# Kernel optimization log

Measured on AMD Instinct MI355X. Metric: run time of the kernel, lower is better.

## Reference

```python
import jax, jax.numpy as jnp
import numpy as np

N_USERS, N_ITEMS = 100000, 100000
N_NODES = N_USERS + N_ITEMS
N_EDGES = 4000000
USER_DIM, ITEM_DIM = 256, 128
COMMON, HIDDEN, OUT = 64, 64, 32


def setup_inputs() -> dict:
    key = jax.random.key(0)
    ks = jax.random.split(key, 12)
    inp = {
        "user_tensor": jax.random.normal(ks[0], (N_USERS, USER_DIM), jnp.float32),
        "item_tensor": jax.random.normal(ks[1], (N_ITEMS, ITEM_DIM), jnp.float32),
        "edge_index": jax.random.randint(ks[2], (2, N_EDGES), 0, N_NODES, jnp.int64),
        "edge_weight": jax.random.uniform(ks[3], (N_EDGES,), jnp.float32),
        # user_proj / item_proj (nn.Linear: y = x @ W + b)
        "Wu": jax.random.normal(ks[4], (USER_DIM, COMMON), jnp.float32) / np.sqrt(USER_DIM),
        "bu": jnp.zeros((COMMON,), jnp.float32),
        "Wi": jax.random.normal(ks[5], (ITEM_DIM, COMMON), jnp.float32) / np.sqrt(ITEM_DIM),
        "bi": jnp.zeros((COMMON,), jnp.float32),
        # GCNConv layers (linear without bias + separate bias)
        "W1": jax.random.normal(ks[6], (COMMON, HIDDEN), jnp.float32) / np.sqrt(COMMON),
        "b1": jnp.zeros((HIDDEN,), jnp.float32),
        "W2": jax.random.normal(ks[7], (HIDDEN, OUT), jnp.float32) / np.sqrt(HIDDEN),
        "b2": jnp.zeros((OUT,), jnp.float32),
    }
    return inp


def gcn_conv(x, W, b, src, dst, ew, num_nodes):
    """PyG GCNConv: add self-loops (weight 1), symmetric deg norm, transform, scatter-add."""
    x = x @ W  # transform first: [N, out]
    loop = jnp.arange(num_nodes, dtype=src.dtype)
    src2 = jnp.concatenate([src, loop])
    dst2 = jnp.concatenate([dst, loop])
    ew2 = jnp.concatenate([ew, jnp.ones((num_nodes,), x.dtype)])
    deg = jax.ops.segment_sum(ew2, dst2, num_segments=num_nodes)
    dinv = jnp.where(deg > 0, jax.lax.rsqrt(deg), 0.0)
    norm = dinv[src2] * ew2 * dinv[dst2]  # [E+N]
    msgs = x[src2] * norm[:, None]  # gather + scale: [E+N, out]
    return jax.ops.segment_sum(msgs, dst2, num_segments=num_nodes) + b


def reference(user_tensor, item_tensor, edge_index, edge_weight,
              Wu, bu, Wi, bi, W1, b1, W2, b2):
    user_emb = user_tensor @ Wu + bu
    item_emb = item_tensor @ Wi + bi
    x = jnp.concatenate([user_emb, item_emb], axis=0)  # [N_NODES, COMMON]
    src, dst = edge_index[0], edge_index[1]
    x = gcn_conv(x, W1, b1, src, dst, edge_weight, N_NODES)
    x = jax.nn.relu(x)
    x = gcn_conv(x, W2, b2, src, dst, edge_weight, N_NODES)
    return x
```

## Files before the change

kernel.cpp:

```cpp
#include <hip/hip_runtime.h>
#include <hip/hip_bf16.h>

#define N_USERS_C 100000
#define N_ITEMS_C 100000
#define N_NODES_C 200000
#define USER_DIM_C 256
#define ITEM_DIM_C 128
#define COMMON_C 64
#define HIDDEN_C 64
#define OUT_DIM_C 32

#define BUCKET_BITS 6
#define BUCKET_NODES 64
#define NBKT (N_NODES_C / BUCKET_NODES)
#define BKT_CAP 1536

#define BIN_GRID 512
#define BIN_CHUNK_MAX 8192
#define MAX_EPT 8

typedef unsigned int uint32;
typedef __bf16 bf16x8 __attribute__((ext_vector_type(8)));
typedef float f32x4 __attribute__((ext_vector_type(4)));



__device__ __forceinline__ float bf2f(ushort u) { return __uint_as_float(((unsigned)u) << 16); }
__device__ __forceinline__ ushort f2bf(float f) {
    unsigned u = __float_as_uint(f);
    return (ushort)((u + 0x7FFFu + ((u >> 16) & 1u)) >> 16);
}
__device__ __forceinline__ void store4(float* p, float a, float b, float c, float d) {
    *(float4*)p = make_float4(a, b, c, d);
}
__device__ __forceinline__ void store4(ushort* p, float a, float b, float c, float d) {
    ushort4 u;
    u.x = f2bf(a); u.y = f2bf(b); u.z = f2bf(c); u.w = f2bf(d);
    *(ushort4*)p = u;
}

union ABFrag {
    uint4 q;
    ushort u[8];
    bf16x8 v;
};


__global__ __launch_bounds__(1024) void bin_kernel(const int* __restrict__ src,
                                                   const int* __restrict__ dst,
                                                   const float* __restrict__ ew,
                                                   int* __restrict__ bucket_cnt,
                                                   uint32* __restrict__ rec, int E, int chunk) {
    __shared__ int hist[NBKT];
    __shared__ int cur[NBKT];
    for (int i = threadIdx.x; i < NBKT; i += 1024) hist[i] = 0;
    __syncthreads();
    const int beg = blockIdx.x * chunk;
    const int end = min(E, beg + chunk);

    int dc[MAX_EPT];
#pragma unroll
    for (int s = 0; s < MAX_EPT / 4; ++s) {
        const int e0 = beg + (threadIdx.x << 2) + (s << 12);
        int4 d4 = make_int4(-1, -1, -1, -1);
        if (e0 + 3 < end) {
            d4 = *(const int4*)(dst + e0);
        } else if (e0 < end) {
            d4.x = dst[e0];
            if (e0 + 1 < end) d4.y = dst[e0 + 1];
            if (e0 + 2 < end) d4.z = dst[e0 + 2];
        }
        dc[s * 4 + 0] = d4.x; dc[s * 4 + 1] = d4.y;
        dc[s * 4 + 2] = d4.z; dc[s * 4 + 3] = d4.w;
        if (d4.x >= 0) atomicAdd(&hist[d4.x >> BUCKET_BITS], 1);
        if (d4.y >= 0) atomicAdd(&hist[d4.y >> BUCKET_BITS], 1);
        if (d4.z >= 0) atomicAdd(&hist[d4.z >> BUCKET_BITS], 1);
        if (d4.w >= 0) atomicAdd(&hist[d4.w >> BUCKET_BITS], 1);
    }
    __syncthreads();

    for (int i = threadIdx.x; i < NBKT; i += 1024) {
        const int h = hist[i];
        cur[i] = h ? atomicAdd(&bucket_cnt[i], h) : 0;
    }
    __syncthreads();

#pragma unroll
    for (int s = 0; s < MAX_EPT / 4; ++s) {
        const int e0 = beg + (threadIdx.x << 2) + (s << 12);
        if (e0 >= end) continue;
        int4 s4;
        float4 w4;
        if (e0 + 3 < end) {
            s4 = *(const int4*)(src + e0);
            w4 = *(const float4*)(ew + e0);
        } else {
            s4 = make_int4(0, 0, 0, 0);
            w4 = make_float4(0, 0, 0, 0);
            s4.x = src[e0]; w4.x = ew[e0];
            if (e0 + 1 < end) { s4.y = src[e0 + 1]; w4.y = ew[e0 + 1]; }
            if (e0 + 2 < end) { s4.z = src[e0 + 2]; w4.z = ew[e0 + 2]; }
        }
        const int dv[4] = {dc[s * 4 + 0], dc[s * 4 + 1], dc[s * 4 + 2], dc[s * 4 + 3]};
        const int sv[4] = {s4.x, s4.y, s4.z, s4.w};
        const float wv[4] = {w4.x, w4.y, w4.z, w4.w};
#pragma unroll
        for (int k = 0; k < 4; ++k) {
            const int d = dv[k];
            if (d < 0) continue;
            uint32 q = (uint32)(wv[k] * 255.0f + 0.5f);
            if (q > 255u) q = 255u;
            const int b = d >> BUCKET_BITS;
            const int slot = atomicAdd(&cur[b], 1);
            if (slot < BKT_CAP)
                rec[(size_t)b * BKT_CAP + slot] =
                    (((uint32)sv[k]) << 14) | (q << 6) | (uint32)(d & (BUCKET_NODES - 1));
        }
    }
}


__global__ void bucket_build_kernel(const uint32* __restrict__ rec,
                                    const int* __restrict__ bucket_cnt,
                                    uint32* __restrict__ csr, int* __restrict__ row_beg,
                                    int* __restrict__ row_cnt, float* __restrict__ dinv) {
    __shared__ int pk[BUCKET_NODES];
    __shared__ int s[BUCKET_NODES];
    __shared__ int cur[BUCKET_NODES];
    const int b = blockIdx.x;
    const int node0 = b << BUCKET_BITS;
    int total = bucket_cnt[b];
    if (total > BKT_CAP) total = BKT_CAP;
    const uint32* r = rec + (size_t)b * BKT_CAP;
    if (threadIdx.x < BUCKET_NODES) pk[threadIdx.x] = 0;
    __syncthreads();
    for (int j0 = threadIdx.x * 4; j0 < total; j0 += 1024) {
        if (j0 + 4 <= total) {
            uint4 r4 = *(const uint4*)(r + j0);
            atomicAdd(&pk[r4.x & (BUCKET_NODES - 1)], (int)((1u << 20) | ((r4.x >> 6) & 255u)));
            atomicAdd(&pk[r4.y & (BUCKET_NODES - 1)], (int)((1u << 20) | ((r4.y >> 6) & 255u)));
            atomicAdd(&pk[r4.z & (BUCKET_NODES - 1)], (int)((1u << 20) | ((r4.z >> 6) & 255u)));
            atomicAdd(&pk[r4.w & (BUCKET_NODES - 1)], (int)((1u << 20) | ((r4.w >> 6) & 255u)));
        } else {
            for (int j = j0; j < total; ++j) {
                uint32 e = r[j];
                atomicAdd(&pk[e & (BUCKET_NODES - 1)], (int)((1u << 20) | ((e >> 6) & 255u)));
            }
        }
    }
    __syncthreads();
    int v = 0;
    if (threadIdx.x < BUCKET_NODES) {
        v = pk[threadIdx.x] >> 20;
        s[threadIdx.x] = v;
    }
    __syncthreads();
#pragma unroll
    for (int off = 1; off < BUCKET_NODES; off <<= 1) {
        int t = (threadIdx.x < BUCKET_NODES && threadIdx.x >= off) ? s[threadIdx.x - off] : 0;
        __syncthreads();
        if (threadIdx.x < BUCKET_NODES) s[threadIdx.x] += t;
        __syncthreads();
    }
    if (threadIdx.x < BUCKET_NODES) {
        const int ex = s[threadIdx.x] - v;
        const int node = node0 + threadIdx.x;
        const int abs0 = b * BKT_CAP + ex;
        row_beg[node] = abs0;
        row_cnt[node] = v;
        dinv[node] = rsqrtf(1.0f + (float)(pk[threadIdx.x] & 0xFFFFF) * (1.0f / 255.0f));
        cur[threadIdx.x] = abs0;
    }
    __syncthreads();
    for (int j0 = threadIdx.x * 4; j0 < total; j0 += 1024) {
        if (j0 + 4 <= total) {
            uint4 r4 = *(const uint4*)(r + j0);
            csr[atomicAdd(&cur[r4.x & (BUCKET_NODES - 1)], 1)] = r4.x;
            csr[atomicAdd(&cur[r4.y & (BUCKET_NODES - 1)], 1)] = r4.y;
            csr[atomicAdd(&cur[r4.z & (BUCKET_NODES - 1)], 1)] = r4.z;
            csr[atomicAdd(&cur[r4.w & (BUCKET_NODES - 1)], 1)] = r4.w;
        } else {
            for (int j = j0; j < total; ++j) {
                uint32 e = r[j];
                csr[atomicAdd(&cur[e & (BUCKET_NODES - 1)], 1)] = e;
            }
        }
    }
}


__device__ __forceinline__ void wt_one(const float* W, ushort* WT, int K, int N, int i) {
    int k = i / N, n = i % N;
    WT[(size_t)n * K + k] = f2bf(W[i]);
}

__global__ void wt_prep_kernel(const float* __restrict__ Wu, const float* __restrict__ Wi,
                               const float* __restrict__ W1, const float* __restrict__ W2,
                               ushort* __restrict__ wtU, ushort* __restrict__ wtI,
                               ushort* __restrict__ wt1, ushort* __restrict__ wt2) {
    const int SU = USER_DIM_C * 64, SI = ITEM_DIM_C * 64, S1 = 64 * 64, S2 = 64 * 32;
    int i = blockIdx.x * blockDim.x + threadIdx.x;
    if (i < SU) { wt_one(Wu, wtU, USER_DIM_C, 64, i); return; }
    i -= SU;
    if (i < SI) { wt_one(Wi, wtI, ITEM_DIM_C, 64, i); return; }
    i -= SI;
    if (i < S1) { wt_one(W1, wt1, 64, 64, i); return; }
    i -= S1;
    if (i < S2) wt_one(W2, wt2, 64, 32, i);
}

template <int K, int NT, bool XF32, bool SCALE>
__global__ __launch_bounds__(256) void mfma_proj_kernel(const void* __restrict__ Xv,
                                                        const ushort* __restrict__ WT,
                                                        const float* __restrict__ bias,
                                                        const float* __restrict__ dinvp,
                                                        ushort* __restrict__ Y, int M) {
    const int lane = threadIdx.x & 63;
    const int wave = threadIdx.x >> 6;
    const int lr = lane & 15;
    const int quad = lane >> 4;
    const int m0 = blockIdx.x * 64 + wave * 16;
    const int N = NT * 16;

    f32x4 acc[NT];
#pragma unroll
    for (int nt = 0; nt < NT; ++nt) acc[nt] = (f32x4){0.0f, 0.0f, 0.0f, 0.0f};

    int arow = m0 + lr;
    if (arow >= M) arow = M - 1;
    const size_t abase = (size_t)arow * K;

    for (int kc = 0; kc < K; kc += 32) {
        const int k0 = kc + quad * 8;
        ABFrag a;
        if (XF32) {
            const float* Xf = (const float*)Xv;
            float4 x0 = *(const float4*)(Xf + abase + k0);
            float4 x1 = *(const float4*)(Xf + abase + k0 + 4);
            a.u[0] = f2bf(x0.x); a.u[1] = f2bf(x0.y); a.u[2] = f2bf(x0.z); a.u[3] = f2bf(x0.w);
            a.u[4] = f2bf(x1.x); a.u[5] = f2bf(x1.y); a.u[6] = f2bf(x1.z); a.u[7] = f2bf(x1.w);
        } else {
            const ushort* Xb = (const ushort*)Xv;
            a.q = *(const uint4*)(Xb + abase + k0);
        }
#pragma unroll
        for (int nt = 0; nt < NT; ++nt) {
            ABFrag bf;
            bf.q = *(const uint4*)(WT + (size_t)(nt * 16 + lr) * K + k0);
            acc[nt] = __builtin_amdgcn_mfma_f32_16x16x32_bf16(a.v, bf.v, acc[nt], 0, 0, 0);
        }
    }

#pragma unroll
    for (int r = 0; r < 4; ++r) {
        const int m = m0 + quad * 4 + r;
        if (m < M) {
            const float sc = SCALE ? dinvp[m] : 1.0f;
#pragma unroll
            for (int nt = 0; nt < NT; ++nt) {
                const int n = nt * 16 + lr;
                const float bc = bias ? bias[n] : 0.0f;
                Y[(size_t)m * N + n] = f2bf((acc[nt][r] + bc) * sc);
            }
        }
    }
}

template <int N, bool RELU, typename TY>
__global__ void gather_kernel(const int* __restrict__ row_beg, const int* __restrict__ row_cnt,
                              const uint32* __restrict__ csr, const ushort* __restrict__ y,
                              const float* __restrict__ dinv, const float* __restrict__ b,
                              TY* __restrict__ out) {
    constexpr int LPN = N / 4;
    const int node = blockIdx.x * (256 / LPN) + threadIdx.x / LPN;
    const int c0 = (threadIdx.x % LPN) * 4;

    const int beg = row_beg[node];
    const int end = beg + row_cnt[node];

    float a0[4] = {0, 0, 0, 0}, a1[4] = {0, 0, 0, 0}, a2[4] = {0, 0, 0, 0}, a3[4] = {0, 0, 0, 0};
    int j = beg;
    for (; j + 4 <= end; j += 4) {
        uint32 e0 = csr[j], e1 = csr[j + 1], e2 = csr[j + 2], e3 = csr[j + 3];
        int s0 = e0 >> 14, s1 = e1 >> 14, s2 = e2 >> 14, s3 = e3 >> 14;
        float c0v = (float)((e0 >> 6) & 255u) * (1.0f / 255.0f);
        float c1v = (float)((e1 >> 6) & 255u) * (1.0f / 255.0f);
        float c2v = (float)((e2 >> 6) & 255u) * (1.0f / 255.0f);
        float c3v = (float)((e3 >> 6) & 255u) * (1.0f / 255.0f);
        ushort4 u0 = *(const ushort4*)(y + (size_t)s0 * N + c0);
        ushort4 u1 = *(const ushort4*)(y + (size_t)s1 * N + c0);
        ushort4 u2 = *(const ushort4*)(y + (size_t)s2 * N + c0);
        ushort4 u3 = *(const ushort4*)(y + (size_t)s3 * N + c0);
        a0[0] += bf2f(u0.x) * c0v; a0[1] += bf2f(u0.y) * c0v;
        a0[2] += bf2f(u0.z) * c0v; a0[3] += bf2f(u0.w) * c0v;
        a1[0] += bf2f(u1.x) * c1v; a1[1] += bf2f(u1.y) * c1v;
        a1[2] += bf2f(u1.z) * c1v; a1[3] += bf2f(u1.w) * c1v;
        a2[0] += bf2f(u2.x) * c2v; a2[1] += bf2f(u2.y) * c2v;
        a2[2] += bf2f(u2.z) * c2v; a2[3] += bf2f(u2.w) * c2v;
        a3[0] += bf2f(u3.x) * c3v; a3[1] += bf2f(u3.y) * c3v;
        a3[2] += bf2f(u3.z) * c3v; a3[3] += bf2f(u3.w) * c3v;
    }
    for (; j < end; ++j) {
        uint32 e = csr[j];
        int s = e >> 14;
        float cv = (float)((e >> 6) & 255u) * (1.0f / 255.0f);
        ushort4 u = *(const ushort4*)(y + (size_t)s * N + c0);
        a0[0] += bf2f(u.x) * cv; a0[1] += bf2f(u.y) * cv;
        a0[2] += bf2f(u.z) * cv; a0[3] += bf2f(u.w) * cv;
    }
    const float di = dinv[node];
    ushort4 us = *(const ushort4*)(y + (size_t)node * N + c0);
    float4 bc = *(const float4*)(b + c0);
    float r0 = (((a0[0] + a1[0]) + (a2[0] + a3[0])) + bf2f(us.x)) * di + bc.x;
    float r1 = (((a0[1] + a1[1]) + (a2[1] + a3[1])) + bf2f(us.y)) * di + bc.y;
    float r2 = (((a0[2] + a1[2]) + (a2[2] + a3[2])) + bf2f(us.z)) * di + bc.z;
    float r3 = (((a0[3] + a1[3]) + (a2[3] + a3[3])) + bf2f(us.w)) * di + bc.w;
    if (RELU) {
        r0 = fmaxf(r0, 0.0f); r1 = fmaxf(r1, 0.0f);
        r2 = fmaxf(r2, 0.0f); r3 = fmaxf(r3, 0.0f);
    }
    store4(&out[(size_t)node * N + c0], r0, r1, r2, r3);
}


extern "C" void kernel_launch(void* const* d_in, const int* in_sizes, int n_in,
                              void* d_out, int out_size, void* d_ws, size_t ws_size,
                              hipStream_t stream) {
    const float* user = (const float*)d_in[0];
    const float* item = (const float*)d_in[1];
    const int* ei = (const int*)d_in[2];
    const float* ew = (const float*)d_in[3];
    const float* Wu = (const float*)d_in[4];
    const float* bu = (const float*)d_in[5];
    const float* Wi = (const float*)d_in[6];
    const float* bi = (const float*)d_in[7];
    const float* W1 = (const float*)d_in[8];
    const float* b1 = (const float*)d_in[9];
    const float* W2 = (const float*)d_in[10];
    const float* b2 = (const float*)d_in[11];
    float* out = (float*)d_out;

    const int E = in_sizes[3];
    const int* src = ei;
    const int* dst = ei + E;
    const int NB = N_NODES_C;
    const int nblk = (E > BIN_GRID * BIN_CHUNK_MAX) ? ((E + BIN_CHUNK_MAX - 1) / BIN_CHUNK_MAX)
                                                    : BIN_GRID;
    const int chunk = (((E + nblk - 1) / nblk) + 3) & ~3;

    char* p = (char*)d_ws;
    uint32* rec = (uint32*)p;  p += (size_t)NBKT * BKT_CAP * 4;
    uint32* csr = (uint32*)p;  p += (size_t)NBKT * BKT_CAP * 4;
    ushort* emb = (ushort*)p;  p += (size_t)NB * 64 * 2;
    ushort* y1 = (ushort*)p;   p += (size_t)NB * 64 * 2;
    ushort* h1 = (ushort*)p;   p += (size_t)NB * 64 * 2;
    ushort* y2 = (ushort*)p;   p += (size_t)NB * 32 * 2;
    int* bucket_cnt = (int*)p; p += (size_t)NBKT * 4;
    int* row_beg = (int*)p;    p += (size_t)NB * 4;
    int* row_cnt = (int*)p;    p += (size_t)NB * 4;
    float* dinv = (float*)p;   p += (size_t)NB * 4;
    ushort* wtU = (ushort*)p;  p += (size_t)USER_DIM_C * 64 * 2;
    ushort* wtI = (ushort*)p;  p += (size_t)ITEM_DIM_C * 64 * 2;
    ushort* wt1 = (ushort*)p;  p += (size_t)64 * 64 * 2;
    ushort* wt2 = (ushort*)p;  p += (size_t)64 * 32 * 2;

    hipMemsetAsync(bucket_cnt, 0, (size_t)NBKT * 4, stream);
    bin_kernel<<<nblk, 1024, 0, stream>>>(src, dst, ew, bucket_cnt, rec, E, chunk);
    bucket_build_kernel<<<NBKT, 256, 0, stream>>>(rec, bucket_cnt, csr, row_beg, row_cnt, dinv);

    wt_prep_kernel<<<120, 256, 0, stream>>>(Wu, Wi, W1, W2, wtU, wtI, wt1, wt2);

    mfma_proj_kernel<USER_DIM_C, 4, true, false><<<(N_USERS_C + 63) / 64, 256, 0, stream>>>(
        user, wtU, bu, nullptr, emb, N_USERS_C);
    mfma_proj_kernel<ITEM_DIM_C, 4, true, false><<<(N_ITEMS_C + 63) / 64, 256, 0, stream>>>(
        item, wtI, bi, nullptr, emb + (size_t)N_USERS_C * 64, N_ITEMS_C);

    mfma_proj_kernel<64, 4, false, true><<<NB / 64, 256, 0, stream>>>(
        emb, wt1, (const float*)nullptr, dinv, y1, NB);
    gather_kernel<64, true><<<NB / 16, 256, 0, stream>>>(row_beg, row_cnt, csr, y1, dinv, b1, h1);

    mfma_proj_kernel<64, 2, false, true><<<NB / 64, 256, 0, stream>>>(
        h1, wt2, (const float*)nullptr, dinv, y2, NB);
    gather_kernel<32, false><<<NB / 32, 256, 0, stream>>>(row_beg, row_cnt, csr, y2, dinv, b2, out);
}
```

Baseline: 540.4 us.

## Use 256-node coarse buckets with in-place register-staged CSR build

Dst bucketing moves from 64-node to 256-node buckets, so the binning kernel's shared histogram shrinks and there are fewer global bucket atomics. Records become 8-byte pairs (src<<8|q, dst). The build kernel keeps each bucket's records in registers and then writes the packed 32-bit CSR over the same buffer, which drops the separate CSR allocation. This reduces shared-memory pressure and the number of build blocks. In exchange, binning writes twice as many bytes, and per-bucket overflow handling depends on the new capacity.

```diff
diff --git a/kernel.cpp b/kernel.cpp
--- a/kernel.cpp
+++ b/kernel.cpp
@@ -10,10 +10,12 @@
 #define HIDDEN_C 64
 #define OUT_DIM_C 32
 
-#define BUCKET_BITS 6
-#define BUCKET_NODES 64
-#define NBKT (N_NODES_C / BUCKET_NODES)
-#define BKT_CAP 1536
+#define CB_BITS 8
+#define CB_NODES 256
+#define NCB ((N_NODES_C + CB_NODES - 1) / CB_NODES)
+#define CB_CAP 5632
+#define B_THREADS 256
+#define B_UNROLL (CB_CAP / B_THREADS)
 
 #define BIN_GRID 512
 #define BIN_CHUNK_MAX 8192
@@ -50,10 +52,10 @@
                                                    const int* __restrict__ dst,
                                                    const float* __restrict__ ew,
                                                    int* __restrict__ bucket_cnt,
-                                                   uint32* __restrict__ rec, int E, int chunk) {
-    __shared__ int hist[NBKT];
-    __shared__ int cur[NBKT];
-    for (int i = threadIdx.x; i < NBKT; i += 1024) hist[i] = 0;
+                                                   uint2* __restrict__ rec2, int E, int chunk) {
+    __shared__ int hist[NCB];
+    __shared__ int cur[NCB];
+    for (int i = threadIdx.x; i < NCB; i += 1024) hist[i] = 0;
     __syncthreads();
     const int beg = blockIdx.x * chunk;
     const int end = min(E, beg + chunk);
@@ -72,14 +74,14 @@
         }
         dc[s * 4 + 0] = d4.x; dc[s * 4 + 1] = d4.y;
         dc[s * 4 + 2] = d4.z; dc[s * 4 + 3] = d4.w;
-        if (d4.x >= 0) atomicAdd(&hist[d4.x >> BUCKET_BITS], 1);
-        if (d4.y >= 0) atomicAdd(&hist[d4.y >> BUCKET_BITS], 1);
-        if (d4.z >= 0) atomicAdd(&hist[d4.z >> BUCKET_BITS], 1);
-        if (d4.w >= 0) atomicAdd(&hist[d4.w >> BUCKET_BITS], 1);
-    }
-    __syncthreads();
-
-    for (int i = threadIdx.x; i < NBKT; i += 1024) {
+        if (d4.x >= 0) atomicAdd(&hist[d4.x >> CB_BITS], 1);
+        if (d4.y >= 0) atomicAdd(&hist[d4.y >> CB_BITS], 1);
+        if (d4.z >= 0) atomicAdd(&hist[d4.z >> CB_BITS], 1);
+        if (d4.w >= 0) atomicAdd(&hist[d4.w >> CB_BITS], 1);
+    }
+    __syncthreads();
+
+    for (int i = threadIdx.x; i < NCB; i += 1024) {
         const int h = hist[i];
         cur[i] = h ? atomicAdd(&bucket_cnt[i], h) : 0;
     }
@@ -110,80 +112,74 @@
             if (d < 0) continue;
             uint32 q = (uint32)(wv[k] * 255.0f + 0.5f);
             if (q > 255u) q = 255u;
-            const int b = d >> BUCKET_BITS;
+            const int b = d >> CB_BITS;
             const int slot = atomicAdd(&cur[b], 1);
-            if (slot < BKT_CAP)
-                rec[(size_t)b * BKT_CAP + slot] =
-                    (((uint32)sv[k]) << 14) | (q << 6) | (uint32)(d & (BUCKET_NODES - 1));
-        }
-    }
-}
-
-
-__global__ void bucket_build_kernel(const uint32* __restrict__ rec,
-                                    const int* __restrict__ bucket_cnt,
-                                    uint32* __restrict__ csr, int* __restrict__ row_beg,
-                                    int* __restrict__ row_cnt, float* __restrict__ dinv) {
-    __shared__ int pk[BUCKET_NODES];
-    __shared__ int s[BUCKET_NODES];
-    __shared__ int cur[BUCKET_NODES];
-    const int b = blockIdx.x;
-    const int node0 = b << BUCKET_BITS;
-    int total = bucket_cnt[b];
-    if (total > BKT_CAP) total = BKT_CAP;
-    const uint32* r = rec + (size_t)b * BKT_CAP;
-    if (threadIdx.x < BUCKET_NODES) pk[threadIdx.x] = 0;
-    __syncthreads();
-    for (int j0 = threadIdx.x * 4; j0 < total; j0 += 1024) {
-        if (j0 + 4 <= total) {
-            uint4 r4 = *(const uint4*)(r + j0);
-            atomicAdd(&pk[r4.x & (BUCKET_NODES - 1)], (int)((1u << 20) | ((r4.x >> 6) & 255u)));
-            atomicAdd(&pk[r4.y & (BUCKET_NODES - 1)], (int)((1u << 20) | ((r4.y >> 6) & 255u)));
-            atomicAdd(&pk[r4.z & (BUCKET_NODES - 1)], (int)((1u << 20) | ((r4.z >> 6) & 255u)));
-            atomicAdd(&pk[r4.w & (BUCKET_NODES - 1)], (int)((1u << 20) | ((r4.w >> 6) & 255u)));
+            if (slot < CB_CAP)
+                rec2[(size_t)b * CB_CAP + slot] =
+                    make_uint2((((uint32)sv[k]) << 8) | q, (uint32)d);
+        }
+    }
+}
+
+
+__global__ __launch_bounds__(B_THREADS) void region_build_kernel(
+        const uint2* __restrict__ rec2, const int* __restrict__ bucket_cnt,
+        uint32* __restrict__ csr32, int* __restrict__ row_beg,
+        int* __restrict__ row_cnt, float* __restrict__ dinv) {
+    __shared__ int pk[CB_NODES];
+    __shared__ int s[CB_NODES];
+    __shared__ int cur[CB_NODES];
+    const int cb = blockIdx.x;
+    const int node0 = cb << CB_BITS;
+    int total = bucket_cnt[cb];
+    if (total > CB_CAP) total = CB_CAP;
+    const uint2* r = rec2 + (size_t)cb * CB_CAP;
+
+    pk[threadIdx.x] = 0;
+    __syncthreads();
+
+    uint2 rr[B_UNROLL];
+#pragma unroll
+    for (int u = 0; u < B_UNROLL; ++u) {
+        const int j = threadIdx.x + u * B_THREADS;
+        if (j < total) {
+            rr[u] = r[j];
+            atomicAdd(&pk[rr[u].y & (CB_NODES - 1)],
+                      (int)((1u << 20) | (rr[u].x & 255u)));
         } else {
-            for (int j = j0; j < total; ++j) {
-                uint32 e = r[j];
-                atomicAdd(&pk[e & (BUCKET_NODES - 1)], (int)((1u << 20) | ((e >> 6) & 255u)));
-            }
-        }
-    }
-    __syncthreads();
-    int v = 0;
-    if (threadIdx.x < BUCKET_NODES) {
-        v = pk[threadIdx.x] >> 20;
-        s[threadIdx.x] = v;
-    }
-    __syncthreads();
-#pragma unroll
-    for (int off = 1; off < BUCKET_NODES; off <<= 1) {
-        int t = (threadIdx.x < BUCKET_NODES && threadIdx.x >= off) ? s[threadIdx.x - off] : 0;
+            rr[u] = make_uint2(0u, 0xFFFFFFFFu);
+        }
+    }
+    __syncthreads();
+
+    const int v = pk[threadIdx.x] >> 20;
+    s[threadIdx.x] = v;
+    __syncthreads();
+#pragma unroll
+    for (int off = 1; off < CB_NODES; off <<= 1) {
+        const int t = (threadIdx.x >= off) ? s[threadIdx.x - off] : 0;
         __syncthreads();
-        if (threadIdx.x < BUCKET_NODES) s[threadIdx.x] += t;
+        s[threadIdx.x] += t;
         __syncthreads();
     }
-    if (threadIdx.x < BUCKET_NODES) {
+    {
         const int ex = s[threadIdx.x] - v;
         const int node = node0 + threadIdx.x;
-        const int abs0 = b * BKT_CAP + ex;
-        row_beg[node] = abs0;
-        row_cnt[node] = v;
-        dinv[node] = rsqrtf(1.0f + (float)(pk[threadIdx.x] & 0xFFFFF) * (1.0f / 255.0f));
+        const int abs0 = cb * (2 * CB_CAP) + ex;
+        if (node < N_NODES_C) {
+            row_beg[node] = abs0;
+            row_cnt[node] = v;
+            dinv[node] = rsqrtf(1.0f + (float)(pk[threadIdx.x] & 0xFFFFF) * (1.0f / 255.0f));
+        }
         cur[threadIdx.x] = abs0;
     }
     __syncthreads();
-    for (int j0 = threadIdx.x * 4; j0 < total; j0 += 1024) {
-        if (j0 + 4 <= total) {
-            uint4 r4 = *(const uint4*)(r + j0);
-            csr[atomicAdd(&cur[r4.x & (BUCKET_NODES - 1)], 1)] = r4.x;
-            csr[atomicAdd(&cur[r4.y & (BUCKET_NODES - 1)], 1)] = r4.y;
-            csr[atomicAdd(&cur[r4.z & (BUCKET_NODES - 1)], 1)] = r4.z;
-            csr[atomicAdd(&cur[r4.w & (BUCKET_NODES - 1)], 1)] = r4.w;
-        } else {
-            for (int j = j0; j < total; ++j) {
-                uint32 e = r[j];
-                csr[atomicAdd(&cur[e & (BUCKET_NODES - 1)], 1)] = e;
-            }
+
+#pragma unroll
+    for (int u = 0; u < B_UNROLL; ++u) {
+        if (rr[u].y != 0xFFFFFFFFu) {
+            const int slot = atomicAdd(&cur[rr[u].y & (CB_NODES - 1)], 1);
+            csr32[slot] = rr[u].x;
         }
     }
 }
@@ -282,11 +278,11 @@
     int j = beg;
     for (; j + 4 <= end; j += 4) {
         uint32 e0 = csr[j], e1 = csr[j + 1], e2 = csr[j + 2], e3 = csr[j + 3];
-        int s0 = e0 >> 14, s1 = e1 >> 14, s2 = e2 >> 14, s3 = e3 >> 14;
-        float c0v = (float)((e0 >> 6) & 255u) * (1.0f / 255.0f);
-        float c1v = (float)((e1 >> 6) & 255u) * (1.0f / 255.0f);
-        float c2v = (float)((e2 >> 6) & 255u) * (1.0f / 255.0f);
-        float c3v = (float)((e3 >> 6) & 255u) * (1.0f / 255.0f);
+        int s0 = e0 >> 8, s1 = e1 >> 8, s2 = e2 >> 8, s3 = e3 >> 8;
+        float c0v = (float)(e0 & 255u) * (1.0f / 255.0f);
+        float c1v = (float)(e1 & 255u) * (1.0f / 255.0f);
+        float c2v = (float)(e2 & 255u) * (1.0f / 255.0f);
+        float c3v = (float)(e3 & 255u) * (1.0f / 255.0f);
         ushort4 u0 = *(const ushort4*)(y + (size_t)s0 * N + c0);
         ushort4 u1 = *(const ushort4*)(y + (size_t)s1 * N + c0);
         ushort4 u2 = *(const ushort4*)(y + (size_t)s2 * N + c0);
@@ -302,8 +298,8 @@
     }
     for (; j < end; ++j) {
         uint32 e = csr[j];
-        int s = e >> 14;
-        float cv = (float)((e >> 6) & 255u) * (1.0f / 255.0f);
+        int s = e >> 8;
+        float cv = (float)(e & 255u) * (1.0f / 255.0f);
         ushort4 u = *(const ushort4*)(y + (size_t)s * N + c0);
         a0[0] += bf2f(u.x) * cv; a0[1] += bf2f(u.y) * cv;
         a0[2] += bf2f(u.z) * cv; a0[3] += bf2f(u.w) * cv;
@@ -349,13 +345,12 @@
     const int chunk = (((E + nblk - 1) / nblk) + 3) & ~3;
 
     char* p = (char*)d_ws;
-    uint32* rec = (uint32*)p;  p += (size_t)NBKT * BKT_CAP * 4;
-    uint32* csr = (uint32*)p;  p += (size_t)NBKT * BKT_CAP * 4;
+    uint2* rec2 = (uint2*)p;   p += (size_t)NCB * CB_CAP * 8;
     ushort* emb = (ushort*)p;  p += (size_t)NB * 64 * 2;
     ushort* y1 = (ushort*)p;   p += (size_t)NB * 64 * 2;
     ushort* h1 = (ushort*)p;   p += (size_t)NB * 64 * 2;
     ushort* y2 = (ushort*)p;   p += (size_t)NB * 32 * 2;
-    int* bucket_cnt = (int*)p; p += (size_t)NBKT * 4;
+    int* bucket_cnt = (int*)p; p += (size_t)NCB * 4;
     int* row_beg = (int*)p;    p += (size_t)NB * 4;
     int* row_cnt = (int*)p;    p += (size_t)NB * 4;
     float* dinv = (float*)p;   p += (size_t)NB * 4;
@@ -364,9 +359,12 @@
     ushort* wt1 = (ushort*)p;  p += (size_t)64 * 64 * 2;
     ushort* wt2 = (ushort*)p;  p += (size_t)64 * 32 * 2;
 
-    hipMemsetAsync(bucket_cnt, 0, (size_t)NBKT * 4, stream);
-    bin_kernel<<<nblk, 1024, 0, stream>>>(src, dst, ew, bucket_cnt, rec, E, chunk);
-    bucket_build_kernel<<<NBKT, 256, 0, stream>>>(rec, bucket_cnt, csr, row_beg, row_cnt, dinv);
+    uint32* csr = (uint32*)rec2;
+
+    hipMemsetAsync(bucket_cnt, 0, (size_t)NCB * 4, stream);
+    bin_kernel<<<nblk, 1024, 0, stream>>>(src, dst, ew, bucket_cnt, rec2, E, chunk);
+    region_build_kernel<<<NCB, B_THREADS, 0, stream>>>(rec2, bucket_cnt, csr, row_beg, row_cnt,
+                                                       dinv);
 
     wt_prep_kernel<<<120, 256, 0, stream>>>(Wu, Wi, W1, W2, wtU, wtI, wt1, wt2);
 
```

After: 526.1 us. 1.03x faster.
